# Kernel optimization log

Hardware: AMD Instinct MI355X
Metric: run time of the kernel (lower is better)

The kernel has to match this reference:

```python
import jax, jax.numpy as jnp
import numpy as np

D, N, L, H, VOCAB = 256, 8192, 6, 4, 256
EPS = 1e-5


def layernorm(x):
    # LayerNorm over last dim, no affine (matches nn.LayerNorm(D, elementwise_affine=False))
    mu = jnp.mean(x, axis=-1, keepdims=True)
    var = jnp.mean(jnp.square(x - mu), axis=-1, keepdims=True)
    return (x - mu) * jax.lax.rsqrt(var + EPS)


def rotate_half(x):
    x1, x2 = jnp.split(x, 2, axis=-1)
    return jnp.concatenate((-x2, x1), axis=-1)


def rope_tables(T, dim, dtype):
    inv_freq = 1.0 / (10000.0 ** (jnp.arange(0, dim, 2, dtype=jnp.float32) / dim))
    t = jnp.arange(T, dtype=jnp.float32)
    freqs = jnp.einsum('i,j->ij', t, inv_freq)          # [T, dim/2]
    emb = jnp.concatenate((freqs, freqs), axis=-1)       # [T, dim]
    return jnp.cos(emb).astype(dtype), jnp.sin(emb).astype(dtype)


def linear_attention(Q, K, V):
    # unnormalized causal attention with RoPE on Q, K
    B, T, d = Q.shape
    cos, sin = rope_tables(T, d, Q.dtype)
    Qr = Q * cos + rotate_half(Q) * sin
    Kr = K * cos + rotate_half(K) * sin
    energy = jnp.einsum('btd,bsd->bts', Qr, Kr)          # [B, T, T]
    mask = jnp.tril(jnp.ones((T, T), dtype=energy.dtype))
    energy = energy * mask
    return jnp.einsum('bts,bsd->btd', energy, V)


def setup_inputs() -> dict:
    key = jax.random.key(0)
    ks = jax.random.split(key, 6)
    idx = jax.random.randint(ks[0], (4, 2048), 0, VOCAB)
    wte = jax.random.normal(ks[1], (VOCAB, D), dtype=jnp.float32) * 0.02
    encoder = jax.random.normal(ks[2], (N, D), dtype=jnp.float32) * 0.02
    decoder_x = jax.random.normal(ks[3], (H, D, N // H), dtype=jnp.float32) * 0.02
    decoder_y = jax.random.normal(ks[4], (H, D, N // H), dtype=jnp.float32) * 0.02
    readout = jax.random.normal(ks[5], (D, VOCAB), dtype=jnp.float32) * 0.02
    return {"idx": idx, "wte": wte, "encoder": encoder,
            "decoder_x": decoder_x, "decoder_y": decoder_y, "readout": readout}


def reference(idx, wte, encoder, decoder_x, decoder_y, readout):
    B, T = idx.shape
    v_ast = layernorm(wte[idx])                          # [B, T, D]
    for _ in range(L):
        x_raw = jnp.einsum('btd,hdm->bthm', v_ast, decoder_x)
        x = jax.nn.relu(x_raw)                           # [B, T, H, N/H]
        a_ast = linear_attention(v_ast, v_ast, v_ast)
        y_raw = jnp.einsum('btd,hdm->bthm', layernorm(a_ast), decoder_y)
        y = jax.nn.relu(y_raw) * x
        y_flat = y.reshape(B, T, -1)                     # [B, T, N]
        update = y_flat @ encoder                        # [B, T, D]
        v_ast = v_ast + layernorm(update)
    logits = v_ast @ readout                             # [B, T, VOCAB]
    return logits
```

## Files before the change

### kernel.cpp

```cpp
#include <hip/hip_runtime.h>
#include <hip/hip_bf16.h>

typedef __hip_bfloat16 bf16;
typedef _Float16 half_t;
typedef __attribute__((ext_vector_type(8))) _Float16 half8;
typedef __attribute__((ext_vector_type(4))) float f32x4;

#define LN_EPS 1e-5f

static constexpr int Dk     = 256;
static constexpr int Tk     = 2048;
static constexpr int BTk    = 8192;
static constexpr int MHk    = 2048;
static constexpr int Nk     = 8192;
static constexpr int LAYERS = 6;
static constexpr long long TD  = (long long)Tk * Dk;
static constexpr long long BTD = (long long)BTk * Dk;
static constexpr long long TT  = (long long)Tk * Tk;

#define SKQ(t) ((((t) & 3) ^ (((t) >> 3) & 3)) * 8)

__device__ __forceinline__ float wave_reduce(float v) {
#pragma unroll
    for (int o = 32; o > 0; o >>= 1) v += __shfl_down(v, o);
    return v;
}

__device__ __forceinline__ float block_sum_256(float x, float* sbuf) {
    float s = wave_reduce(x);
    int lane = threadIdx.x & 63, wv = threadIdx.x >> 6;
    if (lane == 0) sbuf[wv] = s;
    __syncthreads();
    float r = sbuf[0] + sbuf[1] + sbuf[2] + sbuf[3];
    __syncthreads();
    return r;
}

__device__ __forceinline__ void glds16(const void* g, void* lds) {
    __builtin_amdgcn_global_load_lds(
        (const __attribute__((address_space(1))) void*)g,
        (__attribute__((address_space(3))) void*)lds, 16, 0, 0);
}

__device__ __forceinline__ void rope_row(const float* nv, int t, half_t* qrow) {
    int i = threadIdx.x;
    if (i < 128) {
        float invf = powf(10000.f, -(float)i / 128.f);
        float ang = (float)t * invf;
        float s, c;
        sincosf(ang, &s, &c);
        float q1 = nv[i], q2 = nv[128 + i];
        qrow[i]       = (half_t)(q1 * c - q2 * s);
        qrow[128 + i] = (half_t)(q2 * c + q1 * s);
    }
}

__global__ __launch_bounds__(256) void sniff_kernel(const unsigned short* __restrict__ w,
                                                    int* __restrict__ flag) {
    __shared__ float sbuf[4];
    int tid = threadIdx.x;
    float cnt = 0.f;
    for (int i = tid; i < 1024; i += 256) {
        int e = (w[i] >> 7) & 0xFF;
        if (e >= 128) cnt += 1.f;
    }
    float tot = block_sum_256(cnt, sbuf);
    if (tid == 0) *flag = (tot > 32.f) ? 1 : 0;
}

__global__ __launch_bounds__(256) void tr_cvt16_kernel(const void* __restrict__ src,
                                                       const int* __restrict__ flag,
                                                       half_t* __restrict__ dst,
                                                       int R, int C,
                                                       long long sz, long long dz) {
    __shared__ float t[32][33];
    bool f32 = (*flag != 0);
    int ct = blockIdx.x * 32, rt = blockIdx.y * 32;
    long long so = (long long)blockIdx.z * sz, dofs = (long long)blockIdx.z * dz;
    int tx = threadIdx.x & 31, ty = threadIdx.x >> 5;
#pragma unroll
    for (int i = 0; i < 4; i++) {
        long long idx = so + (long long)(rt + ty + i * 8) * C + ct + tx;
        t[ty + i * 8][tx] = f32 ? ((const float*)src)[idx] : (float)((const bf16*)src)[idx];
    }
    __syncthreads();
#pragma unroll
    for (int i = 0; i < 4; i++) {
        long long odx = dofs + (long long)(ct + ty + i * 8) * R + rt + tx;
        dst[odx] = (half_t)t[tx][ty + i * 8];
    }
}

__global__ __launch_bounds__(256) void trv_kernel(const float* __restrict__ src,
                                                  half_t* __restrict__ dst) {
    __shared__ float t[32][33];
    int ct = blockIdx.x * 32, rt = blockIdx.y * 32;
    int tx = threadIdx.x & 31, ty = threadIdx.x >> 5;
#pragma unroll
    for (int i = 0; i < 4; i++)
        t[ty + i * 8][tx] = src[(long long)(rt + ty + i * 8) * Dk + ct + tx];
    __syncthreads();
#pragma unroll
    for (int i = 0; i < 4; i++)
        dst[(long long)(ct + ty + i * 8) * BTk + rt + tx] = (half_t)t[tx][ty + i * 8];
}

__global__ __launch_bounds__(256) void embed_ln_kernel(const int* __restrict__ idx,
                                                       const void* __restrict__ wte,
                                                       const int* __restrict__ flag,
                                                       float* __restrict__ v,
                                                       half_t* __restrict__ vf,
                                                       half_t* __restrict__ qf) {
    __shared__ float sbuf[4];
    __shared__ float nvs[256];
    int bt = blockIdx.x, tid = threadIdx.x;
    int id = idx[bt];
    bool f32 = (*flag != 0);
    float x = f32 ? ((const float*)wte)[id * Dk + tid]
                  : (float)((const bf16*)wte)[id * Dk + tid];
    float mu = block_sum_256(x, sbuf) * (1.f / 256.f);
    float d = x - mu;
    float var = block_sum_256(d * d, sbuf) * (1.f / 256.f);
    float r = d * rsqrtf(var + LN_EPS);
    v[bt * Dk + tid] = r;
    vf[bt * Dk + tid] = (half_t)r;
    nvs[tid] = r;
    __syncthreads();
    rope_row(nvs, bt & (Tk - 1), qf + (long long)bt * Dk);
}

__global__ __launch_bounds__(256) void ln_rows_kernel(const float* __restrict__ Pa,
                                                      half_t* __restrict__ of) {
    __shared__ float sbuf[4];
    int bt = blockIdx.x, tid = threadIdx.x;
    int b = bt >> 11, t = bt & (Tk - 1);
    int ncnt = ((t & ~127) >> 9) + 1;
    const float* p = Pa + ((long long)(b << 2)) * TD + (long long)t * Dk + tid;
    float x = 0.f;
    for (int c = 0; c < ncnt; c++) x += p[(long long)c * TD];
    float mu = block_sum_256(x, sbuf) * (1.f / 256.f);
    float d = x - mu;
    float var = block_sum_256(d * d, sbuf) * (1.f / 256.f);
    float r = d * rsqrtf(var + LN_EPS);
    of[bt * Dk + tid] = (half_t)r;
}

__global__ __launch_bounds__(256) void add_ln_kernel(const float* __restrict__ Pu,
                                                     float* __restrict__ v,
                                                     half_t* __restrict__ vf,
                                                     half_t* __restrict__ qf) {
    __shared__ float sbuf[4];
    __shared__ float nvs[256];
    int bt = blockIdx.x, tid = threadIdx.x;
    long long e = (long long)bt * Dk + tid;
    float x = Pu[e] + Pu[e + BTD] + Pu[e + 2 * BTD] + Pu[e + 3 * BTD];
    float mu = block_sum_256(x, sbuf) * (1.f / 256.f);
    float d = x - mu;
    float var = block_sum_256(d * d, sbuf) * (1.f / 256.f);
    float r = d * rsqrtf(var + LN_EPS);
    float nv = v[e] + r;
    v[e] = nv;
    vf[e] = (half_t)nv;
    nvs[tid] = nv;
    __syncthreads();
    rope_row(nvs, bt & (Tk - 1), qf + (long long)bt * Dk);
}

__global__ __launch_bounds__(256) void gemm128e(
    const half_t* __restrict__ Q, half_t* __restrict__ E) {
    __shared__ __align__(16) half_t As[128 * 32];
    __shared__ __align__(16) half_t Bs[128 * 32];
    const int tid = threadIdx.x;
    const int lane = tid & 63, wv = tid >> 6;
    const int wr = wv >> 1, wc = wv & 1;
    const int quad = lane >> 4, r = lane & 15;
    const int qsw = (quad ^ ((r >> 1) & 3)) * 8;
    const int mb = blockIdx.y * 128, nb = blockIdx.x * 128;
    if ((int)blockIdx.x > (int)blockIdx.y) return;
    const half_t* Qb = Q + (long long)blockIdx.z * TD;
    half_t* Eb = E + (long long)blockIdx.z * TT;

    f32x4 acc[4][4] = {};
    const int srow = tid >> 2, skq = SKQ(tid);
    const int wbase = (tid & 192) * 8;
    for (int k0 = 0; k0 < Dk; k0 += 32) {
#pragma unroll
        for (int rnd = 0; rnd < 2; rnd++) {
            int row = rnd * 64 + srow;
            glds16(Qb + (long long)(mb + row) * Dk + k0 + skq, As + rnd * 2048 + wbase);
            glds16(Qb + (long long)(nb + row) * Dk + k0 + skq, Bs + rnd * 2048 + wbase);
        }
        __syncthreads();
        half8 bfr[4];
#pragma unroll
        for (int ni = 0; ni < 4; ni++)
            bfr[ni] = *(const half8*)&Bs[(wc * 64 + ni * 16 + r) * 32 + qsw];
#pragma unroll
        for (int mi = 0; mi < 4; mi++) {
            half8 afr = *(const half8*)&As[(wr * 64 + mi * 16 + r) * 32 + qsw];
#pragma unroll
            for (int ni = 0; ni < 4; ni++)
                acc[mi][ni] = __builtin_amdgcn_mfma_f32_16x16x32_f16(afr, bfr[ni], acc[mi][ni], 0, 0, 0);
        }
        __syncthreads();
    }
#pragma unroll
    for (int mi = 0; mi < 4; mi++)
#pragma unroll
        for (int ni = 0; ni < 4; ni++) {
            int row0 = mb + wr * 64 + mi * 16 + quad * 4;
            int col = nb + wc * 64 + ni * 16 + r;
#pragma unroll
            for (int rr = 0; rr < 4; rr++) {
                int row = row0 + rr;
                float val = (row < col) ? 0.f : acc[mi][ni][rr];
                Eb[(long long)row * Tk + col] = (half_t)val;
            }
        }
}

__global__ __launch_bounds__(256) void gemm128a(
    const half_t* __restrict__ E, const half_t* __restrict__ vT,
    float* __restrict__ Pa) {
    __shared__ __align__(16) half_t As[128 * 32];
    __shared__ __align__(16) half_t Bs[128 * 32];
    const int tid = threadIdx.x;
    const int lane = tid & 63, wv = tid >> 6;
    const int wr = wv >> 1, wc = wv & 1;
    const int quad = lane >> 4, r = lane & 15;
    const int qsw = (quad ^ ((r >> 1) & 3)) * 8;
    const int mb = blockIdx.x * 128, nb = blockIdx.y * 128;
    const int b = blockIdx.z >> 2, c = blockIdx.z & 3;
    const int kbeg = c * 512;
    const int kend = min(mb + 128, kbeg + 512);
    if (kend <= kbeg) return;

    const half_t* Ab = E + (long long)b * TT;
    const half_t* Bb = vT + (long long)b * Tk;
    float* Pc = Pa + (long long)blockIdx.z * TD;
    f32x4 acc[4][4] = {};
    const int srow = tid >> 2, skq = SKQ(tid);
    const int wbase = (tid & 192) * 8;
    for (int k0 = kbeg; k0 < kend; k0 += 32) {
#pragma unroll
        for (int rnd = 0; rnd < 2; rnd++) {
            int row = rnd * 64 + srow;
            glds16(Ab + (long long)(mb + row) * Tk + k0 + skq, As + rnd * 2048 + wbase);
            glds16(Bb + (long long)(nb + row) * BTk + k0 + skq, Bs + rnd * 2048 + wbase);
        }
        __syncthreads();
        half8 bfr[4];
#pragma unroll
        for (int ni = 0; ni < 4; ni++)
            bfr[ni] = *(const half8*)&Bs[(wc * 64 + ni * 16 + r) * 32 + qsw];
#pragma unroll
        for (int mi = 0; mi < 4; mi++) {
            half8 afr = *(const half8*)&As[(wr * 64 + mi * 16 + r) * 32 + qsw];
#pragma unroll
            for (int ni = 0; ni < 4; ni++)
                acc[mi][ni] = __builtin_amdgcn_mfma_f32_16x16x32_f16(afr, bfr[ni], acc[mi][ni], 0, 0, 0);
        }
        __syncthreads();
    }
#pragma unroll
    for (int mi = 0; mi < 4; mi++)
#pragma unroll
        for (int ni = 0; ni < 4; ni++) {
            int row0 = mb + wr * 64 + mi * 16 + quad * 4;
            int col = nb + wc * 64 + ni * 16 + r;
#pragma unroll
            for (int rr = 0; rr < 4; rr++)
                Pc[(long long)(row0 + rr) * Dk + col] = acc[mi][ni][rr];
        }
}

__global__ __launch_bounds__(256, 2) void dual_gemm(
    const half_t* __restrict__ A1,
    const half_t* __restrict__ A2,
    const half_t* __restrict__ dxT,
    const half_t* __restrict__ dyT,
    half_t* __restrict__ C) {
    __shared__ __align__(16) half_t As1[128 * 64];
    __shared__ __align__(16) half_t As2[128 * 64];
    __shared__ __align__(16) half_t Bs1[128 * 64];
    __shared__ __align__(16) half_t Bs2[128 * 64];
    const int tid = threadIdx.x;
    const int lane = tid & 63, wv = tid >> 6;
    const int wr = wv >> 1, wc = wv & 1;
    const int quad = lane >> 4, r = lane & 15;
    const int flat = blockIdx.x + 16 * (blockIdx.y + 64 * blockIdx.z);
    const int xcd = flat & 7, j = flat >> 3;
    const int mt = (xcd >> 2) * 32 + (j >> 4);
    const int nt = (xcd & 3) * 4 + (j & 3);
    const int h  = (j >> 2) & 3;
    const int mb = mt * 128, nb = nt * 128;
    const half_t* B1 = dxT + (long long)h * MHk * Dk;
    const half_t* B2 = dyT + (long long)h * MHk * Dk;

    f32x4 accX[4][4] = {};
    f32x4 accY[4][4] = {};
    const int srow8 = lane >> 3;
    const int soct  = (lane & 7) ^ srow8;
    for (int k0 = 0; k0 < Dk; k0 += 64) {
#pragma unroll
        for (int c = 0; c < 4; c++) {
            int row = wv * 32 + c * 8;
            long long ga = (long long)(mb + row + srow8) * Dk + k0 + soct * 8;
            long long gb = (long long)(nb + row + srow8) * Dk + k0 + soct * 8;
            glds16(A1 + ga, As1 + row * 64);
            glds16(A2 + ga, As2 + row * 64);
            glds16(B1 + gb, Bs1 + row * 64);
            glds16(B2 + gb, Bs2 + row * 64);
        }
        __syncthreads();
#pragma unroll
        for (int sub = 0; sub < 2; sub++) {
            half8 b1f[4], b2f[4];
#pragma unroll
            for (int ni = 0; ni < 4; ni++) {
                int R = wc * 64 + ni * 16 + r;
                int pos = ((sub * 4 + quad) ^ (R & 7)) * 8;
                b1f[ni] = *(const half8*)&Bs1[R * 64 + pos];
                b2f[ni] = *(const half8*)&Bs2[R * 64 + pos];
            }
#pragma unroll
            for (int mi = 0; mi < 4; mi++) {
                int R = wr * 64 + mi * 16 + r;
                int pos = ((sub * 4 + quad) ^ (R & 7)) * 8;
                half8 a1 = *(const half8*)&As1[R * 64 + pos];
                half8 a2 = *(const half8*)&As2[R * 64 + pos];
#pragma unroll
                for (int ni = 0; ni < 4; ni++) {
                    accX[mi][ni] = __builtin_amdgcn_mfma_f32_16x16x32_f16(a1, b1f[ni], accX[mi][ni], 0, 0, 0);
                    accY[mi][ni] = __builtin_amdgcn_mfma_f32_16x16x32_f16(a2, b2f[ni], accY[mi][ni], 0, 0, 0);
                }
            }
        }
        __syncthreads();
    }
#pragma unroll
    for (int mi = 0; mi < 4; mi++)
#pragma unroll
        for (int ni = 0; ni < 4; ni++) {
            int row0 = mb + wr * 64 + mi * 16 + quad * 4;
            int col = h * MHk + nb + wc * 64 + ni * 16 + r;
#pragma unroll
            for (int rr = 0; rr < 4; rr++) {
                float val = fmaxf(accY[mi][ni][rr], 0.f) * fmaxf(accX[mi][ni][rr], 0.f);
                C[(long long)(row0 + rr) * Nk + col] = (half_t)val;
            }
        }
}

__global__ __launch_bounds__(256, 2) void gemm128u(
    const half_t* __restrict__ A, const half_t* __restrict__ B,
    float* __restrict__ Pu) {
    __shared__ __align__(16) half_t As[4][128 * 32];
    __shared__ __align__(16) half_t Bs[4][128 * 32];
    const int tid = threadIdx.x;
    const int lane = tid & 63, wv = tid >> 6;
    const int wr = wv >> 1, wc = wv & 1;
    const int quad = lane >> 4, r = lane & 15;
    const int qsw = (quad ^ ((r >> 1) & 3)) * 8;
    const int flat = blockIdx.x;
    const int xcd = flat & 7, j = flat >> 3;
    const int nb = (j & 1) * 128;
    const int kc = (j >> 1) & 3;
    const int mb = (xcd * 8 + (j >> 3)) * 128;
    const int kbeg = kc * 2048;
    float* Pc = Pu + (long long)kc * BTD;

    f32x4 acc[4][4] = {};
    const int srow = tid >> 2, skq = SKQ(tid);
    const int wbase = (tid & 192) * 8;

    auto stage = [&](int ks) {
        const int k0 = kbeg + ks * 32;
        const int bsel = ks & 3;
#pragma unroll
        for (int rnd = 0; rnd < 2; rnd++) {
            int row = rnd * 64 + srow;
            glds16(A + (long long)(mb + row) * Nk + k0 + skq, &As[bsel][rnd * 2048 + wbase]);
            glds16(B + (long long)(nb + row) * Nk + k0 + skq, &Bs[bsel][rnd * 2048 + wbase]);
        }
    };
    auto compute = [&](int ks) {
        const int cur = ks & 3;
        half8 bfr[4];
#pragma unroll
        for (int ni = 0; ni < 4; ni++)
            bfr[ni] = *(const half8*)&Bs[cur][(wc * 64 + ni * 16 + r) * 32 + qsw];
#pragma unroll
        for (int mi = 0; mi < 4; mi++) {
            half8 afr = *(const half8*)&As[cur][(wr * 64 + mi * 16 + r) * 32 + qsw];
#pragma unroll
            for (int ni = 0; ni < 4; ni++)
                acc[mi][ni] = __builtin_amdgcn_mfma_f32_16x16x32_f16(afr, bfr[ni], acc[mi][ni], 0, 0, 0);
        }
    };

    stage(0); stage(1); stage(2);
    for (int ks = 0; ks < 61; ks++) {
        asm volatile("s_waitcnt vmcnt(8)" ::: "memory");
        __builtin_amdgcn_s_barrier();
        __builtin_amdgcn_sched_barrier(0);
        stage(ks + 3);
        __builtin_amdgcn_s_setprio(1);
        compute(ks);
        __builtin_amdgcn_s_setprio(0);
    }
    asm volatile("s_waitcnt vmcnt(8)" ::: "memory");
    __builtin_amdgcn_s_barrier();
    __builtin_amdgcn_sched_barrier(0);
    compute(61);
    asm volatile("s_waitcnt vmcnt(4)" ::: "memory");
    __builtin_amdgcn_s_barrier();
    __builtin_amdgcn_sched_barrier(0);
    compute(62);
    asm volatile("s_waitcnt vmcnt(0)" ::: "memory");
    __builtin_amdgcn_s_barrier();
    __builtin_amdgcn_sched_barrier(0);
    compute(63);

#pragma unroll
    for (int mi = 0; mi < 4; mi++)
#pragma unroll
        for (int ni = 0; ni < 4; ni++) {
            int row0 = mb + wr * 64 + mi * 16 + quad * 4;
            int col = nb + wc * 64 + ni * 16 + r;
#pragma unroll
            for (int rr = 0; rr < 4; rr++)
                Pc[(long long)(row0 + rr) * Dk + col] = acc[mi][ni][rr];
        }
}

__global__ __launch_bounds__(256) void gemm64h(
    const half_t* __restrict__ A, int lda,
    const half_t* __restrict__ B, int ldb,
    float* __restrict__ C, int ldc, int K) {
    __shared__ __align__(16) half_t As[64 * 32];
    __shared__ __align__(16) half_t Bs[64 * 32];
    const int tid = threadIdx.x;
    const int lane = tid & 63, wv = tid >> 6;
    const int wr = wv >> 1, wc = wv & 1;
    const int quad = lane >> 4, r = lane & 15;
    const int qsw = (quad ^ ((r >> 1) & 3)) * 8;
    const int mb = blockIdx.y * 64, nb = blockIdx.x * 64;

    f32x4 acc[2][2] = {};
    const int srow = tid >> 2, skq = SKQ(tid);
    const int wbase = (tid & 192) * 8;
    for (int k0 = 0; k0 < K; k0 += 32) {
        glds16(A + (long long)(mb + srow) * lda + k0 + skq, As + wbase);
        glds16(B + (long long)(nb + srow) * ldb + k0 + skq, Bs + wbase);
        __syncthreads();
        half8 b0 = *(const half8*)&Bs[(wc * 32 +  0 + r) * 32 + qsw];
        half8 b1 = *(const half8*)&Bs[(wc * 32 + 16 + r) * 32 + qsw];
#pragma unroll
        for (int mi = 0; mi < 2; mi++) {
            half8 afr = *(const half8*)&As[(wr * 32 + mi * 16 + r) * 32 + qsw];
            acc[mi][0] = __builtin_amdgcn_mfma_f32_16x16x32_f16(afr, b0, acc[mi][0], 0, 0, 0);
            acc[mi][1] = __builtin_amdgcn_mfma_f32_16x16x32_f16(afr, b1, acc[mi][1], 0, 0, 0);
        }
        __syncthreads();
    }
#pragma unroll
    for (int mi = 0; mi < 2; mi++)
#pragma unroll
        for (int ni = 0; ni < 2; ni++) {
            int row0 = mb + wr * 32 + mi * 16 + quad * 4;
            int col = nb + wc * 32 + ni * 16 + r;
#pragma unroll
            for (int rr = 0; rr < 4; rr++)
                C[(long long)(row0 + rr) * ldc + col] = acc[mi][ni][rr];
        }
}

extern "C" void kernel_launch(void* const* d_in, const int* in_sizes, int n_in,
                              void* d_out, int out_size, void* d_ws, size_t ws_size,
                              hipStream_t stream) {
    (void)in_sizes; (void)n_in; (void)out_size; (void)ws_size;
    const int* idx = (const int*)d_in[0];
    float* out = (float*)d_out;

    char* ws = (char*)d_ws;
    float*  v32  = (float*) (ws);
    half_t* vf   = (half_t*)(ws + (  8ll << 20));
    half_t* qf   = (half_t*)(ws + ( 12ll << 20));
    half_t* vT   = (half_t*)(ws + ( 16ll << 20));
    half_t* lnf  = (half_t*)(ws + ( 20ll << 20));
    half_t* E    = (half_t*)(ws + ( 24ll << 20));
    float*  Pa   = (float*) (ws + ( 56ll << 20));
    float*  Pu   = (float*) (ws + ( 24ll << 20));
    half_t* y16  = (half_t*)(ws + ( 88ll << 20));
    half_t* dxT  = (half_t*)(ws + (216ll << 20));
    half_t* dyT  = (half_t*)(ws + (220ll << 20));
    half_t* eT   = (half_t*)(ws + (224ll << 20));
    half_t* roT  = (half_t*)(ws + (228ll << 20));
    int*    flag = (int*)   (ws + (228ll << 20) + (256ll << 10));

    sniff_kernel<<<1, 256, 0, stream>>>((const unsigned short*)d_in[1], flag);
    tr_cvt16_kernel<<<dim3(MHk / 32, Dk / 32, 4), 256, 0, stream>>>(
        d_in[3], flag, dxT, Dk, MHk, (long long)Dk * MHk, (long long)Dk * MHk);
    tr_cvt16_kernel<<<dim3(MHk / 32, Dk / 32, 4), 256, 0, stream>>>(
        d_in[4], flag, dyT, Dk, MHk, (long long)Dk * MHk, (long long)Dk * MHk);
    tr_cvt16_kernel<<<dim3(Dk / 32, Nk / 32, 1), 256, 0, stream>>>(
        d_in[2], flag, eT, Nk, Dk, 0, 0);
    tr_cvt16_kernel<<<dim3(Dk / 32, Dk / 32, 1), 256, 0, stream>>>(
        d_in[5], flag, roT, Dk, Dk, 0, 0);

    embed_ln_kernel<<<BTk, 256, 0, stream>>>(idx, d_in[1], flag, v32, vf, qf);

    for (int l = 0; l < LAYERS; l++) {
        trv_kernel<<<dim3(Dk / 32, BTk / 32), 256, 0, stream>>>(v32, vT);
        gemm128e<<<dim3(Tk / 128, Tk / 128, 4), 256, 0, stream>>>(qf, E);
        gemm128a<<<dim3(Tk / 128, Dk / 128, 16), 256, 0, stream>>>(E, vT, Pa);
        ln_rows_kernel<<<BTk, 256, 0, stream>>>(Pa, lnf);
        dual_gemm<<<dim3(MHk / 128, BTk / 128, 4), 256, 0, stream>>>(
            vf, lnf, dxT, dyT, y16);
        gemm128u<<<dim3(512), 256, 0, stream>>>(y16, eT, Pu);
        add_ln_kernel<<<BTk, 256, 0, stream>>>(Pu, v32, vf, qf);
    }
    gemm64h<<<dim3(Dk / 64, BTk / 64), 256, 0, stream>>>(
        vf, Dk, roT, Dk, out, Dk, Dk);
}
```

Measured before the change: 1.250 ms.

## Multi-stage LDS pipeline for attention GEMMs with async global-to-LDS prefetch

Both attention GEMM kernels (energy and energy·V) now use a 4-buffer shared-memory ring, keeping three k-stages of global-to-LDS loads in flight. Each step waits on the load counter, issues one barrier, then launches the next load. This replaces the two syncthreads per k-step and is meant to hide global load latency behind the MFMA work. LDS per block grows fourfold to 64 KB, so occupancy is capped at two blocks. Correctness relies on hand-written vmcnt wait counts and on a single barrier protecting buffer reuse.

```diff
diff --git a/kernel.cpp b/kernel.cpp
--- a/kernel.cpp
+++ b/kernel.cpp
@@ -166,10 +166,10 @@
     rope_row(nvs, bt & (Tk - 1), qf + (long long)bt * Dk);
 }
 
-__global__ __launch_bounds__(256) void gemm128e(
+__global__ __launch_bounds__(256, 2) void gemm128e(
     const half_t* __restrict__ Q, half_t* __restrict__ E) {
-    __shared__ __align__(16) half_t As[128 * 32];
-    __shared__ __align__(16) half_t Bs[128 * 32];
+    __shared__ __align__(16) half_t As[4][128 * 32];
+    __shared__ __align__(16) half_t Bs[4][128 * 32];
     const int tid = threadIdx.x;
     const int lane = tid & 63, wv = tid >> 6;
     const int wr = wv >> 1, wc = wv & 1;
@@ -183,27 +183,55 @@
     f32x4 acc[4][4] = {};
     const int srow = tid >> 2, skq = SKQ(tid);
     const int wbase = (tid & 192) * 8;
-    for (int k0 = 0; k0 < Dk; k0 += 32) {
+
+    auto stage = [&](int ks) {
+        const int k0 = ks * 32;
+        const int bsel = ks & 3;
 #pragma unroll
         for (int rnd = 0; rnd < 2; rnd++) {
             int row = rnd * 64 + srow;
-            glds16(Qb + (long long)(mb + row) * Dk + k0 + skq, As + rnd * 2048 + wbase);
-            glds16(Qb + (long long)(nb + row) * Dk + k0 + skq, Bs + rnd * 2048 + wbase);
-        }
-        __syncthreads();
+            glds16(Qb + (long long)(mb + row) * Dk + k0 + skq, &As[bsel][rnd * 2048 + wbase]);
+            glds16(Qb + (long long)(nb + row) * Dk + k0 + skq, &Bs[bsel][rnd * 2048 + wbase]);
+        }
+    };
+    auto compute = [&](int ks) {
+        const int cur = ks & 3;
         half8 bfr[4];
 #pragma unroll
         for (int ni = 0; ni < 4; ni++)
-            bfr[ni] = *(const half8*)&Bs[(wc * 64 + ni * 16 + r) * 32 + qsw];
+            bfr[ni] = *(const half8*)&Bs[cur][(wc * 64 + ni * 16 + r) * 32 + qsw];
 #pragma unroll
         for (int mi = 0; mi < 4; mi++) {
-            half8 afr = *(const half8*)&As[(wr * 64 + mi * 16 + r) * 32 + qsw];
+            half8 afr = *(const half8*)&As[cur][(wr * 64 + mi * 16 + r) * 32 + qsw];
 #pragma unroll
             for (int ni = 0; ni < 4; ni++)
                 acc[mi][ni] = __builtin_amdgcn_mfma_f32_16x16x32_f16(afr, bfr[ni], acc[mi][ni], 0, 0, 0);
         }
-        __syncthreads();
-    }
+    };
+
+    stage(0); stage(1); stage(2);
+    for (int ks = 0; ks < 5; ks++) {
+        asm volatile("s_waitcnt vmcnt(8)" ::: "memory");
+        __builtin_amdgcn_s_barrier();
+        __builtin_amdgcn_sched_barrier(0);
+        stage(ks + 3);
+        __builtin_amdgcn_s_setprio(1);
+        compute(ks);
+        __builtin_amdgcn_s_setprio(0);
+    }
+    asm volatile("s_waitcnt vmcnt(8)" ::: "memory");
+    __builtin_amdgcn_s_barrier();
+    __builtin_amdgcn_sched_barrier(0);
+    compute(5);
+    asm volatile("s_waitcnt vmcnt(4)" ::: "memory");
+    __builtin_amdgcn_s_barrier();
+    __builtin_amdgcn_sched_barrier(0);
+    compute(6);
+    asm volatile("s_waitcnt vmcnt(0)" ::: "memory");
+    __builtin_amdgcn_s_barrier();
+    __builtin_amdgcn_sched_barrier(0);
+    compute(7);
+
 #pragma unroll
     for (int mi = 0; mi < 4; mi++)
 #pragma unroll
@@ -219,11 +247,11 @@
         }
 }
 
-__global__ __launch_bounds__(256) void gemm128a(
+__global__ __launch_bounds__(256, 2) void gemm128a(
     const half_t* __restrict__ E, const half_t* __restrict__ vT,
     float* __restrict__ Pa) {
-    __shared__ __align__(16) half_t As[128 * 32];
-    __shared__ __align__(16) half_t Bs[128 * 32];
+    __shared__ __align__(16) half_t As[4][128 * 32];
+    __shared__ __align__(16) half_t Bs[4][128 * 32];
     const int tid = threadIdx.x;
     const int lane = tid & 63, wv = tid >> 6;
     const int wr = wv >> 1, wc = wv & 1;
@@ -234,6 +262,7 @@
     const int kbeg = c * 512;
     const int kend = min(mb + 128, kbeg + 512);
     if (kend <= kbeg) return;
+    const int NS = (kend - kbeg) >> 5;
 
     const half_t* Ab = E + (long long)b * TT;
     const half_t* Bb = vT + (long long)b * Tk;
@@ -241,27 +270,48 @@
     f32x4 acc[4][4] = {};
     const int srow = tid >> 2, skq = SKQ(tid);
     const int wbase = (tid & 192) * 8;
-    for (int k0 = kbeg; k0 < kend; k0 += 32) {
+
+    auto stage = [&](int ks) {
+        const int k0 = kbeg + ks * 32;
+        const int bsel = ks & 3;
 #pragma unroll
         for (int rnd = 0; rnd < 2; rnd++) {
             int row = rnd * 64 + srow;
-            glds16(Ab + (long long)(mb + row) * Tk + k0 + skq, As + rnd * 2048 + wbase);
-            glds16(Bb + (long long)(nb + row) * BTk + k0 + skq, Bs + rnd * 2048 + wbase);
-        }
-        __syncthreads();
+            glds16(Ab + (long long)(mb + row) * Tk + k0 + skq, &As[bsel][rnd * 2048 + wbase]);
+            glds16(Bb + (long long)(nb + row) * BTk + k0 + skq, &Bs[bsel][rnd * 2048 + wbase]);
+        }
+    };
+    auto compute = [&](int ks) {
+        const int cur = ks & 3;
         half8 bfr[4];
 #pragma unroll
         for (int ni = 0; ni < 4; ni++)
-            bfr[ni] = *(const half8*)&Bs[(wc * 64 + ni * 16 + r) * 32 + qsw];
+            bfr[ni] = *(const half8*)&Bs[cur][(wc * 64 + ni * 16 + r) * 32 + qsw];
 #pragma unroll
         for (int mi = 0; mi < 4; mi++) {
-            half8 afr = *(const half8*)&As[(wr * 64 + mi * 16 + r) * 32 + qsw];
+            half8 afr = *(const half8*)&As[cur][(wr * 64 + mi * 16 + r) * 32 + qsw];
 #pragma unroll
             for (int ni = 0; ni < 4; ni++)
                 acc[mi][ni] = __builtin_amdgcn_mfma_f32_16x16x32_f16(afr, bfr[ni], acc[mi][ni], 0, 0, 0);
         }
-        __syncthreads();
-    }
+    };
+
+    stage(0);
+    if (NS > 1) stage(1);
+    if (NS > 2) stage(2);
+    for (int ks = 0; ks < NS; ks++) {
+        const int rem = NS - 1 - ks;
+        if (rem >= 2)      asm volatile("s_waitcnt vmcnt(8)" ::: "memory");
+        else if (rem == 1) asm volatile("s_waitcnt vmcnt(4)" ::: "memory");
+        else               asm volatile("s_waitcnt vmcnt(0)" ::: "memory");
+        __builtin_amdgcn_s_barrier();
+        __builtin_amdgcn_sched_barrier(0);
+        if (ks + 3 < NS) stage(ks + 3);
+        __builtin_amdgcn_s_setprio(1);
+        compute(ks);
+        __builtin_amdgcn_s_setprio(0);
+    }
+
 #pragma unroll
     for (int mi = 0; mi < 4; mi++)
 #pragma unroll
```

Measured after the change: 1.303 ms. +4.3%, slower.
